# Performance work log

Measured on AMD Instinct MI355X. Metric: run time of the kernel, lower is better.

The kernel has to match this reference:

```python
import jax, jax.numpy as jnp
import numpy as np

H, W = 256, 256          # heat_map_shape
P = 512                  # number of ground-truth points
ALPHA = -5.0             # soft-min exponent


def setup_inputs() -> dict:
    key = jax.random.key(0)
    k1, k2 = jax.random.split(key)
    heat_map = jax.random.uniform(k1, (H, W), dtype=jnp.float32)  # values in [0,1]
    # points in [0,H) x [0,W), float coords (never exactly on grid -> dist > 0)
    points = jax.random.uniform(k2, (P, 2), dtype=jnp.float32) * jnp.array([H, W], jnp.float32)
    return {"heat_map": heat_map, "points": points}


def reference(heat_map, points):
    # grid: (H, W, 2) with torch.meshgrid 'ij' indexing semantics
    ys = jnp.arange(H, dtype=jnp.float32)
    xs = jnp.arange(W, dtype=jnp.float32)
    grid = jnp.stack(jnp.meshgrid(ys, xs, indexing="ij"), axis=-1)

    delta = grid[:, :, None, :] - points[None, None]          # (H, W, P, 2)
    dist = jnp.sqrt(jnp.sum(delta * delta, axis=-1))          # (H, W, P)

    # term 1: heatmap-weighted min distance, normalized by L1 norm of heatmap
    weighted_min = jnp.sum(heat_map * jnp.min(dist, axis=-1)) / jnp.sum(jnp.abs(heat_map))

    # term 2: generalized (power) mean soft-min over spatial dims, then mean over P
    hm = heat_map[..., None]                                  # (H, W, 1)
    weighted_dist = hm * dist + (1.0 - hm) * jnp.max(dist)    # (H, W, P)
    soft_min = jnp.mean(weighted_dist ** ALPHA, axis=(0, 1)) ** (1.0 / ALPHA)  # (P,)
    mean_soft_min = jnp.mean(soft_min)

    return weighted_min + mean_soft_min
```

## Files before the change

kernel.cpp:

```cpp
#include <hip/hip_runtime.h>

#define HH 256
#define WW 256
#define NPIX (HH * WW)
#define NP 512

#define PPB 4
#define SLICE_ROWS 32
#define NSLICES (HH / SLICE_ROWS)
#define NPGRP (NP / PPB)
#define NB_T2 (NPGRP * NSLICES)
#define NB_T1 (NPIX / 256)
#define NB_TOTAL (NB_T1 + NB_T2)

#define WS_SUM1 0
#define WS_SUM2 1
#define WS_S    2

__global__ __launch_bounds__(256) void whd_main(const float* __restrict__ hm,
                                                const float* __restrict__ pts,
                                                float* __restrict__ ws) {
    const int tid = threadIdx.x;
    const int bid = blockIdx.x;
    __shared__ float sred[PPB][4];
    __shared__ float dred[4];

    if (bid < NB_T1) {
        const int idx = bid * 256 + tid;
        const float fi = (float)(idx >> 8);
        const float fj = (float)(idx & (WW - 1));
        const float4* pts4 = (const float4*)pts;
        float m0 = 3.4e38f, m1 = 3.4e38f, m2 = 3.4e38f, m3 = 3.4e38f;
        #pragma unroll 4
        for (int i = 0; i < NP / 2; i += 4) {
            float4 q0 = pts4[i], q1 = pts4[i + 1], q2 = pts4[i + 2], q3 = pts4[i + 3];
            float dy, dx;
            dy = fi - q0.x; dx = fj - q0.y; m0 = fminf(m0, fmaf(dy, dy, dx * dx));
            dy = fi - q0.z; dx = fj - q0.w; m1 = fminf(m1, fmaf(dy, dy, dx * dx));
            dy = fi - q1.x; dx = fj - q1.y; m2 = fminf(m2, fmaf(dy, dy, dx * dx));
            dy = fi - q1.z; dx = fj - q1.w; m3 = fminf(m3, fmaf(dy, dy, dx * dx));
            dy = fi - q2.x; dx = fj - q2.y; m0 = fminf(m0, fmaf(dy, dy, dx * dx));
            dy = fi - q2.z; dx = fj - q2.w; m1 = fminf(m1, fmaf(dy, dy, dx * dx));
            dy = fi - q3.x; dx = fj - q3.y; m2 = fminf(m2, fmaf(dy, dy, dx * dx));
            dy = fi - q3.z; dx = fj - q3.w; m3 = fminf(m3, fmaf(dy, dy, dx * dx));
        }
        float mind = __builtin_amdgcn_sqrtf(fminf(fminf(m0, m1), fminf(m2, m3)));
        float h  = hm[idx];
        float v1 = h * mind;
        float v2 = fabsf(h);
        #pragma unroll
        for (int off = 32; off; off >>= 1) {
            v1 += __shfl_down(v1, off, 64);
            v2 += __shfl_down(v2, off, 64);
        }
        if ((tid & 63) == 0) { sred[0][tid >> 6] = v1; sred[1][tid >> 6] = v2; }
        __syncthreads();
        if (tid == 0) atomicAdd(&ws[WS_SUM1], sred[0][0] + sred[0][1] + sred[0][2] + sred[0][3]);
        if (tid == 1) atomicAdd(&ws[WS_SUM2], sred[1][0] + sred[1][1] + sred[1][2] + sred[1][3]);
    } else {
        const int b2 = bid - NB_T1;
        float m = 0.f;
        #pragma unroll
        for (int t = 0; t < 2; ++t) {
            int p = tid + t * 256;
            float py = pts[2 * p], px = pts[2 * p + 1];
            float my = fmaxf(py * py, (255.f - py) * (255.f - py));
            float mx = fmaxf(px * px, (255.f - px) * (255.f - px));
            m = fmaxf(m, my + mx);
        }
        #pragma unroll
        for (int off = 32; off; off >>= 1) m = fmaxf(m, __shfl_down(m, off, 64));
        if ((tid & 63) == 0) dred[tid >> 6] = m;
        __syncthreads();
        const float dmax = __builtin_amdgcn_sqrtf(
            fmaxf(fmaxf(dred[0], dred[1]), fmaxf(dred[2], dred[3])));

        const int pgrp  = b2 & (NPGRP - 1);
        const int slice = b2 >> 7;
        const int p0    = pgrp * PPB;

        float py[PPB], px[PPB];
        #pragma unroll
        for (int a = 0; a < PPB; ++a) {
            py[a] = pts[2 * (p0 + a)];
            px[a] = pts[2 * (p0 + a) + 1];
        }

        const float col0 = (float)((tid & 63) << 2);
        float dx2[PPB][4];
        #pragma unroll
        for (int a = 0; a < PPB; ++a)
            #pragma unroll
            for (int c = 0; c < 4; ++c) {
                float dx = col0 + (float)c - px[a];
                dx2[a][c] = dx * dx;
            }

        const float4* hm4 = (const float4*)hm;
        const int   gbase   = slice * (SLICE_ROWS * WW / 4) + tid;
        const float rowbase = (float)(slice * SLICE_ROWS + (tid >> 6));
        float acc[PPB] = {0.f, 0.f, 0.f, 0.f};

        #pragma unroll
        for (int k = 0; k < 8; ++k) {
            float4 h4 = hm4[gbase + k * 256];
            const float row = rowbase + (float)(4 * k);
            const float hx[4] = {h4.x, h4.y, h4.z, h4.w};
            float ct[4];
            #pragma unroll
            for (int c = 0; c < 4; ++c) ct[c] = fmaf(-hx[c], dmax, dmax);

            #pragma unroll
            for (int a = 0; a < PPB; ++a) {
                float dy = row - py[a];
                float dy2 = dy * dy;
                float w0 = fmaf(hx[0], __builtin_amdgcn_sqrtf(dy2 + dx2[a][0]), ct[0]);
                float w1 = fmaf(hx[1], __builtin_amdgcn_sqrtf(dy2 + dx2[a][1]), ct[1]);
                float w2 = fmaf(hx[2], __builtin_amdgcn_sqrtf(dy2 + dx2[a][2]), ct[2]);
                float w3 = fmaf(hx[3], __builtin_amdgcn_sqrtf(dy2 + dx2[a][3]), ct[3]);
                float p1 = w0 * w1;
                float p2 = p1 * w2;
                float p3 = p2 * w3;
                float r  = __builtin_amdgcn_rcpf(p3);
                float i3 = r * p2;
                float q  = r * w3;
                float i2 = q * p1;
                float q2 = q * w2;
                float i1 = q2 * w0;
                float i0 = q2 * w1;
                float t;
                t = i0 * i0; acc[a] = fmaf(t * t, i0, acc[a]);
                t = i1 * i1; acc[a] = fmaf(t * t, i1, acc[a]);
                t = i2 * i2; acc[a] = fmaf(t * t, i2, acc[a]);
                t = i3 * i3; acc[a] = fmaf(t * t, i3, acc[a]);
            }
        }

        #pragma unroll
        for (int a = 0; a < PPB; ++a) {
            float v = acc[a];
            #pragma unroll
            for (int off = 32; off; off >>= 1) v += __shfl_down(v, off, 64);
            if ((tid & 63) == 0) sred[a][tid >> 6] = v;
        }
        __syncthreads();
        if (tid < PPB) {
            float s = sred[tid][0] + sred[tid][1] + sred[tid][2] + sred[tid][3];
            atomicAdd(&ws[WS_S + p0 + tid], s);
        }
    }
}

__global__ __launch_bounds__(NP) void whd_final(const float* __restrict__ ws,
                                                float* __restrict__ out) {
    const int t = threadIdx.x;
    float S = ws[WS_S + t];
    float sm = exp2f(-0.2f * log2f(S * (1.f / (float)NPIX)));
    #pragma unroll
    for (int off = 32; off; off >>= 1) sm += __shfl_down(sm, off, 64);
    __shared__ float red[8];
    if ((t & 63) == 0) red[t >> 6] = sm;
    __syncthreads();
    if (t == 0) {
        float s = 0.f;
        #pragma unroll
        for (int w = 0; w < 8; ++w) s += red[w];
        out[0] = ws[WS_SUM1] / ws[WS_SUM2] + s * (1.f / (float)NP);
    }
}

extern "C" void kernel_launch(void* const* d_in, const int* in_sizes, int n_in,
                              void* d_out, int out_size, void* d_ws, size_t ws_size,
                              hipStream_t stream) {
    const float* hm  = (const float*)d_in[0];
    const float* pts = (const float*)d_in[1];
    float* ws  = (float*)d_ws;
    float* out = (float*)d_out;

    (void)hipMemsetAsync(d_ws, 0, (WS_S + NP) * sizeof(float), stream);

    whd_main <<<NB_TOTAL, 256, 0, stream>>>(hm, pts, ws);
    whd_final<<<1,        NP,  0, stream>>>(ws, out);
}
```

Before: 77.50 us.

## Replace atomics with per-block partial writes and drop workspace memset

Per-block partial sums are now written to dedicated workspace slots instead of being atomically accumulated. The final kernel reduces those partials, which removes the hipMemsetAsync launch and the atomic contention. The batched reciprocal trick (one rcp shared across four values) is also replaced with one rcp per pixel, which cuts multiplies but adds rcp instructions. The result becomes deterministic. The final kernel does a bit more reading.

```diff
diff --git a/kernel.cpp b/kernel.cpp
--- a/kernel.cpp
+++ b/kernel.cpp
@@ -13,9 +13,9 @@
 #define NB_T1 (NPIX / 256)
 #define NB_TOTAL (NB_T1 + NB_T2)
 
-#define WS_SUM1 0
-#define WS_SUM2 1
-#define WS_S    2
+#define WS_SP   0
+#define WS_T1A  (NP * NSLICES)
+#define WS_T1B  (WS_T1A + NB_T1)
 
 __global__ __launch_bounds__(256) void whd_main(const float* __restrict__ hm,
                                                 const float* __restrict__ pts,
@@ -55,8 +55,8 @@
         }
         if ((tid & 63) == 0) { sred[0][tid >> 6] = v1; sred[1][tid >> 6] = v2; }
         __syncthreads();
-        if (tid == 0) atomicAdd(&ws[WS_SUM1], sred[0][0] + sred[0][1] + sred[0][2] + sred[0][3]);
-        if (tid == 1) atomicAdd(&ws[WS_SUM2], sred[1][0] + sred[1][1] + sred[1][2] + sred[1][3]);
+        if (tid == 0) ws[WS_T1A + bid] = sred[0][0] + sred[0][1] + sred[0][2] + sred[0][3];
+        if (tid == 1) ws[WS_T1B + bid] = sred[1][0] + sred[1][1] + sred[1][2] + sred[1][3];
     } else {
         const int b2 = bid - NB_T1;
         float m = 0.f;
@@ -109,30 +109,20 @@
             float ct[4];
             #pragma unroll
             for (int c = 0; c < 4; ++c) ct[c] = fmaf(-hx[c], dmax, dmax);
+            float dy2[PPB];
+            #pragma unroll
+            for (int a = 0; a < PPB; ++a) { float dy = row - py[a]; dy2[a] = dy * dy; }
 
             #pragma unroll
             for (int a = 0; a < PPB; ++a) {
-                float dy = row - py[a];
-                float dy2 = dy * dy;
-                float w0 = fmaf(hx[0], __builtin_amdgcn_sqrtf(dy2 + dx2[a][0]), ct[0]);
-                float w1 = fmaf(hx[1], __builtin_amdgcn_sqrtf(dy2 + dx2[a][1]), ct[1]);
-                float w2 = fmaf(hx[2], __builtin_amdgcn_sqrtf(dy2 + dx2[a][2]), ct[2]);
-                float w3 = fmaf(hx[3], __builtin_amdgcn_sqrtf(dy2 + dx2[a][3]), ct[3]);
-                float p1 = w0 * w1;
-                float p2 = p1 * w2;
-                float p3 = p2 * w3;
-                float r  = __builtin_amdgcn_rcpf(p3);
-                float i3 = r * p2;
-                float q  = r * w3;
-                float i2 = q * p1;
-                float q2 = q * w2;
-                float i1 = q2 * w0;
-                float i0 = q2 * w1;
-                float t;
-                t = i0 * i0; acc[a] = fmaf(t * t, i0, acc[a]);
-                t = i1 * i1; acc[a] = fmaf(t * t, i1, acc[a]);
-                t = i2 * i2; acc[a] = fmaf(t * t, i2, acc[a]);
-                t = i3 * i3; acc[a] = fmaf(t * t, i3, acc[a]);
+                #pragma unroll
+                for (int c = 0; c < 4; ++c) {
+                    float d  = __builtin_amdgcn_sqrtf(dy2[a] + dx2[a][c]);
+                    float w  = fmaf(hx[c], d, ct[c]);
+                    float r  = __builtin_amdgcn_rcpf(w);
+                    float r2 = r * r;
+                    acc[a]   = fmaf(r2 * r2, r, acc[a]);
+                }
             }
         }
 
@@ -145,8 +135,8 @@
         }
         __syncthreads();
         if (tid < PPB) {
-            float s = sred[tid][0] + sred[tid][1] + sred[tid][2] + sred[tid][3];
-            atomicAdd(&ws[WS_S + p0 + tid], s);
+            ws[WS_SP + (p0 + tid) * NSLICES + slice] =
+                sred[tid][0] + sred[tid][1] + sred[tid][2] + sred[tid][3];
         }
     }
 }
@@ -154,18 +144,27 @@
 __global__ __launch_bounds__(NP) void whd_final(const float* __restrict__ ws,
                                                 float* __restrict__ out) {
     const int t = threadIdx.x;
-    float S = ws[WS_S + t];
+    const float4* w4 = (const float4*)(ws + WS_SP);
+    float4 a = w4[t * 2], b = w4[t * 2 + 1];
+    float S = ((a.x + a.y) + (a.z + a.w)) + ((b.x + b.y) + (b.z + b.w));
     float sm = exp2f(-0.2f * log2f(S * (1.f / (float)NPIX)));
+    float v1 = (t < NB_T1) ? ws[WS_T1A + t] : 0.f;
+    float v2 = (t < NB_T1) ? ws[WS_T1B + t] : 0.f;
+
     #pragma unroll
-    for (int off = 32; off; off >>= 1) sm += __shfl_down(sm, off, 64);
-    __shared__ float red[8];
-    if ((t & 63) == 0) red[t >> 6] = sm;
+    for (int off = 32; off; off >>= 1) {
+        sm += __shfl_down(sm, off, 64);
+        v1 += __shfl_down(v1, off, 64);
+        v2 += __shfl_down(v2, off, 64);
+    }
+    __shared__ float red[3][8];
+    if ((t & 63) == 0) { int w = t >> 6; red[0][w] = sm; red[1][w] = v1; red[2][w] = v2; }
     __syncthreads();
     if (t == 0) {
-        float s = 0.f;
+        float rsm = 0.f, r1 = 0.f, r2 = 0.f;
         #pragma unroll
-        for (int w = 0; w < 8; ++w) s += red[w];
-        out[0] = ws[WS_SUM1] / ws[WS_SUM2] + s * (1.f / (float)NP);
+        for (int w = 0; w < 8; ++w) { rsm += red[0][w]; r1 += red[1][w]; r2 += red[2][w]; }
+        out[0] = r1 / r2 + rsm * (1.f / (float)NP);
     }
 }
 
@@ -177,8 +176,6 @@
     float* ws  = (float*)d_ws;
     float* out = (float*)d_out;
 
-    (void)hipMemsetAsync(d_ws, 0, (WS_S + NP) * sizeof(float), stream);
-
     whd_main <<<NB_TOTAL, 256, 0, stream>>>(hm, pts, ws);
     whd_final<<<1,        NP,  0, stream>>>(ws, out);
 }
```

After: 70.47 us. 1.1x faster.
